# Kernel optimization log

Measured on AMD Instinct MI355X. Metric: run time of the kernel, lower is better.

Reference implementation:

```python
import jax, jax.numpy as jnp
import numpy as np

B, N, C, H, M = 2, 32768, 256, 8, 64
D = C // H  # 32
EPS = 1e-5


def layernorm(x, g, b):
    mu = x.mean(-1, keepdims=True)
    var = ((x - mu) ** 2).mean(-1, keepdims=True)
    return (x - mu) * jax.lax.rsqrt(var + EPS) * g + b


def setup_inputs() -> dict:
    key = jax.random.key(0)
    ks = jax.random.split(key, 12)
    def w(k, shape, fan_in):
        return jax.random.normal(k, shape, jnp.float32) / np.sqrt(fan_in)
    return {
        "x": jax.random.normal(ks[0], (B, N, C), jnp.float32),
        "ln1_g": jnp.ones((C,), jnp.float32),
        "ln1_b": jnp.zeros((C,), jnp.float32),
        "Wfx": w(ks[1], (C, C), C), "bfx": jnp.zeros((C,), jnp.float32),
        "Wx": w(ks[2], (C, C), C), "bx": jnp.zeros((C,), jnp.float32),
        "Wsl": w(ks[3], (D, M), D), "bsl": jnp.zeros((M,), jnp.float32),
        "temp": jnp.full((1, H, 1, 1), 0.5, jnp.float32),
        "Wq": w(ks[4], (D, D), D),
        "Wk": w(ks[5], (D, D), D),
        "Wv": w(ks[6], (D, D), D),
        "Wo": w(ks[7], (C, C), C), "bo": jnp.zeros((C,), jnp.float32),
        "ln2_g": jnp.ones((C,), jnp.float32),
        "ln2_b": jnp.zeros((C,), jnp.float32),
        "W1": w(ks[8], (C, 4 * C), C), "b1": jnp.zeros((4 * C,), jnp.float32),
        "W2": w(ks[9], (4 * C, C), 4 * C), "b2": jnp.zeros((C,), jnp.float32),
    }


def reference(x, ln1_g, ln1_b, Wfx, bfx, Wx, bx, Wsl, bsl, temp,
              Wq, Wk, Wv, Wo, bo, ln2_g, ln2_b, W1, b1, W2, b2):
    scale = D ** -0.5
    h = layernorm(x, ln1_g, ln1_b)
    # projections -> (B,H,N,D)
    fx_mid = (h @ Wfx + bfx).reshape(B, N, H, D).transpose(0, 2, 1, 3)
    x_mid = (h @ Wx + bx).reshape(B, N, H, D).transpose(0, 2, 1, 3)
    # slice routing: (B,H,N,M)
    logits = (x_mid @ Wsl + bsl) / jnp.clip(temp, 0.1, None)
    sw = jax.nn.softmax(logits, axis=-1)
    slice_norm = jnp.clip(sw.sum(axis=2), 1e-5, None)  # (B,H,M)
    slice_token = jnp.einsum('bhnd,bhnm->bhmd', fx_mid, sw) / slice_norm[..., None]
    # small attention over M slices
    q = slice_token @ Wq
    k = slice_token @ Wk
    v = slice_token @ Wv
    attn = jax.nn.softmax(jnp.einsum('bhmd,bhgd->bhmg', q, k) * scale, axis=-1)
    out_slice = jnp.einsum('bhmg,bhgd->bhmd', attn, v)
    # scatter back to N tokens
    out = jnp.einsum('bhmd,bhnm->bhnd', out_slice, sw)
    out = out.transpose(0, 2, 1, 3).reshape(B, N, C) @ Wo + bo
    x = x + out
    h2 = layernorm(x, ln2_g, ln2_b)
    ffn = jax.nn.gelu(h2 @ W1 + b1, approximate=False) @ W2 + b2
    return x + ffn
```

## Files before the change

### kernel.cpp

```cpp
#include <hip/hip_runtime.h>
#include <hip/hip_bf16.h>

typedef float f32x4 __attribute__((ext_vector_type(4)));
typedef short bf16x8 __attribute__((ext_vector_type(8)));
typedef short short4v __attribute__((ext_vector_type(4)));

constexpr int kB = 2, kN = 32768, kC = 256, kH = 8, kD = 32, kM = 64;
constexpr int kT = kB * kN;

__device__ __forceinline__ float b2f(short s) {
    unsigned u = ((unsigned)(unsigned short)s) << 16;
    return __builtin_bit_cast(float, u);
}
__device__ __forceinline__ short f2b(float f) {
    __hip_bfloat16 h = __float2bfloat16(f);
    return __builtin_bit_cast(short, h);
}
__device__ __forceinline__ float gelu_fast(float x) {
    float x2 = x * x;
    float g2 = x * (2.3022042f + 0.10295342f * x2);
#if __has_builtin(__builtin_amdgcn_exp2f)
    float em = __builtin_amdgcn_exp2f(-g2);
#else
    float em = exp2f(-g2);
#endif
#if __has_builtin(__builtin_amdgcn_rcpf)
    return x * __builtin_amdgcn_rcpf(1.0f + em);
#else
    return x / (1.0f + em);
#endif
}

#if __has_builtin(__builtin_amdgcn_global_load_lds)
__device__ __forceinline__ void gld16(const void* g, void* l) {
    __builtin_amdgcn_global_load_lds((__attribute__((address_space(1))) void*)g,
                                     (__attribute__((address_space(3))) void*)l, 16, 0, 0);
}
#else
__device__ __forceinline__ void gld16(const void* g, void* l) {
    *(bf16x8*)l = *(const bf16x8*)g;
}
#endif

__global__ __launch_bounds__(256) void prep_wt(const float* __restrict__ W,
                                               short* __restrict__ Wt, int K, int N) {
    __shared__ float t[32][33];
    int k0 = blockIdx.x * 32, n0 = blockIdx.y * 32;
    int tx = threadIdx.x & 31, ty = threadIdx.x >> 5;
#pragma unroll
    for (int r = 0; r < 32; r += 8)
        t[ty + r][tx] = W[(size_t)(k0 + ty + r) * N + n0 + tx];
    __syncthreads();
#pragma unroll
    for (int r = 0; r < 32; r += 8)
        Wt[(size_t)(n0 + ty + r) * K + k0 + tx] = f2b(t[tx][ty + r]);
}

__global__ __launch_bounds__(256) void prep_pack(const short* __restrict__ src,
                                                 short* __restrict__ dst, int K, int KT) {
    int g = blockIdx.x * 256 + threadIdx.x;
    int frag = g >> 6, lane = g & 63;
    int nt = frag / KT, kt = frag - nt * KT;
    const short* s = &src[(size_t)(nt * 16 + (lane & 15)) * K + kt * 32 + (lane >> 4) * 8];
    *(bf16x8*)&dst[(size_t)frag * 512 + lane * 8] = *(const bf16x8*)s;
}

__global__ __launch_bounds__(256) void prep_wxsl(const float* __restrict__ Wx,
                                                 const float* __restrict__ Wsl,
                                                 const float* __restrict__ bx,
                                                 const float* __restrict__ bsl,
                                                 short* __restrict__ wxsl_t,
                                                 float* __restrict__ bxsl) {
    int n = blockIdx.x;
    int h = n >> 6, m = n & 63;
    int c = threadIdx.x;
    float s = 0.f;
#pragma unroll 8
    for (int dd = 0; dd < 32; ++dd)
        s += Wx[(size_t)c * 256 + h * 32 + dd] * Wsl[dd * 64 + m];
    wxsl_t[(size_t)n * 256 + c] = f2b(s);
    if (c == 0) {
        float bs = bsl[m];
        for (int dd = 0; dd < 32; ++dd) bs += bx[h * 32 + dd] * Wsl[dd * 64 + m];
        bxsl[n] = bs;
    }
}

template <bool IN_BF16>
__global__ __launch_bounds__(256) void ln_kernel(const void* __restrict__ xin,
                                                 const float* __restrict__ g,
                                                 const float* __restrict__ bb,
                                                 short* __restrict__ out) {
    int row = blockIdx.x * 4 + (threadIdx.x >> 6);
    int lane = threadIdx.x & 63;
    float v[4];
    if constexpr (IN_BF16) {
        short4v s = *((const short4v*)((const short*)xin + (size_t)row * kC) + lane);
#pragma unroll
        for (int j = 0; j < 4; ++j) v[j] = b2f(s[j]);
    } else {
        f32x4 s = *((const f32x4*)((const float*)xin + (size_t)row * kC) + lane);
#pragma unroll
        for (int j = 0; j < 4; ++j) v[j] = s[j];
    }
    float sum = v[0] + v[1] + v[2] + v[3];
#pragma unroll
    for (int o = 32; o; o >>= 1) sum += __shfl_xor(sum, o);
    float mu = sum * (1.0f / 256.0f);
    float c[4];
    float s2 = 0.f;
#pragma unroll
    for (int j = 0; j < 4; ++j) { c[j] = v[j] - mu; s2 += c[j] * c[j]; }
#pragma unroll
    for (int o = 32; o; o >>= 1) s2 += __shfl_xor(s2, o);
    float inv = rsqrtf(s2 * (1.0f / 256.0f) + 1e-5f);
    f32x4 gv = *((const f32x4*)g + lane);
    f32x4 bv = *((const f32x4*)bb + lane);
    short4v o;
#pragma unroll
    for (int j = 0; j < 4; ++j) o[j] = f2b(c[j] * inv * gv[j] + bv[j]);
    *((short4v*)(out + (size_t)row * kC) + lane) = o;
}

__global__ __launch_bounds__(256) void wo_gemm(const short* __restrict__ A,
                                               const short* __restrict__ Bt,
                                               const float* __restrict__ bias,
                                               const float* __restrict__ res,
                                               short* __restrict__ Cout) {
    __shared__ __align__(16) short smem[2 * 128 * 64];
    short* As = smem;
    short* Bs = smem + 128 * 64;
    const int tid = threadIdx.x;
    const int lane = tid & 63;
    const int w = tid >> 6, wr = w >> 1, wc = w & 1;
    const int bm = blockIdx.x * 128, bn = blockIdx.y * 128;
    const int l15 = lane & 15, l16 = lane >> 4;
    f32x4 acc[4][4] = {};
    for (int k0 = 0; k0 < 256; k0 += 64) {
        __syncthreads();
#pragma unroll
        for (int l = 0; l < 4; ++l) {
            int li = tid + l * 256;
            int r = li >> 3, s = li & 7;
            int kof = k0 + ((s ^ (r & 7)) << 3);
            gld16(&A[(size_t)(bm + r) * 256 + kof], &As[li * 8]);
            gld16(&Bt[(size_t)(bn + r) * 256 + kof], &Bs[li * 8]);
        }
        __syncthreads();
#pragma unroll
        for (int ks = 0; ks < 2; ++ks) {
            bf16x8 av[4], bv[4];
            int q = ks * 4 + l16;
#pragma unroll
            for (int mi = 0; mi < 4; ++mi) {
                int row = wr * 64 + mi * 16 + l15;
                av[mi] = *(const bf16x8*)(&As[row * 64 + ((q ^ (row & 7)) << 3)]);
            }
#pragma unroll
            for (int ni = 0; ni < 4; ++ni) {
                int row = wc * 64 + ni * 16 + l15;
                bv[ni] = *(const bf16x8*)(&Bs[row * 64 + ((q ^ (row & 7)) << 3)]);
            }
#pragma unroll
            for (int mi = 0; mi < 4; ++mi)
#pragma unroll
                for (int ni = 0; ni < 4; ++ni)
                    acc[mi][ni] = __builtin_amdgcn_mfma_f32_16x16x32_bf16(
                        av[mi], bv[ni], acc[mi][ni], 0, 0, 0);
        }
    }
    __syncthreads();
    char* cs = (char*)smem;
#pragma unroll
    for (int mi = 0; mi < 4; ++mi)
#pragma unroll
        for (int ni = 0; ni < 4; ++ni) {
            int col = wc * 64 + ni * 16 + l15;
            float bcol = bias[bn + col];
#pragma unroll
            for (int r = 0; r < 4; ++r) {
                int row = wr * 64 + mi * 16 + l16 * 4 + r;
                float v = acc[mi][ni][r] + bcol +
                          res[(size_t)(bm + row) * 256 + bn + col];
                *(short*)(cs + row * 256 + ((col * 2) ^ ((row & 7) << 4))) = f2b(v);
            }
        }
    __syncthreads();
#pragma unroll
    for (int pass = 0; pass < 8; ++pass) {
        int row = pass * 16 + (tid >> 4), chunk = tid & 15;
        bf16x8 v = *(const bf16x8*)(cs + row * 256 + ((chunk * 16) ^ ((row & 7) << 4)));
        *(bf16x8*)&Cout[(size_t)(bm + row) * 256 + bn + chunk * 8] = v;
    }
}

__global__ __launch_bounds__(256) void proj_dual(const short* __restrict__ A,
                                                 const short* __restrict__ Bt,
                                                 const float* __restrict__ bfx,
                                                 const float* __restrict__ bxsl,
                                                 short* __restrict__ fxout,
                                                 short* __restrict__ Lout) {
    __shared__ __align__(16) short smem[2 * 128 * 64];
    short* As = smem;
    short* Bs = smem + 128 * 64;
    const int tid = threadIdx.x;
    const int lane = tid & 63;
    const int w = tid >> 6, wr = w >> 1, wc = w & 1;
    const int bm = blockIdx.x * 128, bn = blockIdx.y * 128;
    const int l15 = lane & 15, l16 = lane >> 4;
    f32x4 acc[4][4] = {};
    for (int k0 = 0; k0 < 256; k0 += 64) {
        __syncthreads();
#pragma unroll
        for (int l = 0; l < 4; ++l) {
            int li = tid + l * 256;
            int r = li >> 3, s = li & 7;
            int kof = k0 + ((s ^ (r & 7)) << 3);
            gld16(&A[(size_t)(bm + r) * 256 + kof], &As[li * 8]);
            gld16(&Bt[(size_t)(bn + r) * 256 + kof], &Bs[li * 8]);
        }
        __syncthreads();
#pragma unroll
        for (int ks = 0; ks < 2; ++ks) {
            bf16x8 av[4], bv[4];
            int q = ks * 4 + l16;
#pragma unroll
            for (int mi = 0; mi < 4; ++mi) {
                int row = wr * 64 + mi * 16 + l15;
                av[mi] = *(const bf16x8*)(&As[row * 64 + ((q ^ (row & 7)) << 3)]);
            }
#pragma unroll
            for (int ni = 0; ni < 4; ++ni) {
                int row = wc * 64 + ni * 16 + l15;
                bv[ni] = *(const bf16x8*)(&Bs[row * 64 + ((q ^ (row & 7)) << 3)]);
            }
#pragma unroll
            for (int mi = 0; mi < 4; ++mi)
#pragma unroll
                for (int ni = 0; ni < 4; ++ni)
                    acc[mi][ni] = __builtin_amdgcn_mfma_f32_16x16x32_bf16(
                        av[mi], bv[ni], acc[mi][ni], 0, 0, 0);
        }
    }
    __syncthreads();
    char* cs = (char*)smem;
#pragma unroll
    for (int mi = 0; mi < 4; ++mi)
#pragma unroll
        for (int ni = 0; ni < 4; ++ni) {
            int col = wc * 64 + ni * 16 + l15;
            int gcol = bn + col;
            float bcol = (gcol < 256) ? bfx[gcol] : bxsl[gcol - 256];
#pragma unroll
            for (int r = 0; r < 4; ++r) {
                int row = wr * 64 + mi * 16 + l16 * 4 + r;
                *(short*)(cs + row * 256 + ((col * 2) ^ ((row & 7) << 4))) =
                    f2b(acc[mi][ni][r] + bcol);
            }
        }
    __syncthreads();
    const bool isfx = (bn < 256);
#pragma unroll
    for (int pass = 0; pass < 8; ++pass) {
        int row = pass * 16 + (tid >> 4), chunk = tid & 15;
        bf16x8 v = *(const bf16x8*)(cs + row * 256 + ((chunk * 16) ^ ((row & 7) << 4)));
        if (isfx)
            *(bf16x8*)&fxout[(size_t)(bm + row) * 256 + bn + chunk * 8] = v;
        else
            *(bf16x8*)&Lout[(size_t)(bm + row) * 512 + (bn - 256) + chunk * 8] = v;
    }
}

__global__ __launch_bounds__(256, 2) void ffn_fused(const short* __restrict__ h2,
                                                    const short* __restrict__ xres,
                                                    const short* __restrict__ w1p,
                                                    const short* __restrict__ w2p,
                                                    const float* __restrict__ b1,
                                                    const float* __restrict__ b2,
                                                    float* __restrict__ out) {
    __shared__ __align__(16) short As[64 * 256];
    __shared__ __align__(16) short mids[2][64 * 128];
    const int tid = threadIdx.x;
    const int lane = tid & 63, w = tid >> 6;
    const int l15 = lane & 15, l16 = lane >> 4;
    const int bm = blockIdx.x * 64;
#pragma unroll
    for (int l = 0; l < 8; ++l) {
        int li = tid + l * 256;
        int r = li >> 5, s = li & 31;
        gld16(&h2[(size_t)(bm + r) * 256 + ((s ^ (r & 7)) << 3)], &As[li * 8]);
    }
    __syncthreads();
    f32x4 acc2[4][4] = {};
    f32x4 accm[2][4];

#define FFN_GEMM1(jc)                                                                     \
    {                                                                                     \
        _Pragma("unroll") for (int tj = 0; tj < 4; ++tj) {                                \
            accm[0][tj] = f32x4{0.f, 0.f, 0.f, 0.f};                                      \
            accm[1][tj] = f32x4{0.f, 0.f, 0.f, 0.f};                                      \
        }                                                                                 \
        const short* wp0 = &w1p[(size_t)(((jc)*8 + w * 2) * 8) * 512 + lane * 8];         \
        _Pragma("unroll") for (int ks = 0; ks < 8; ++ks) {                                \
            bf16x8 aw0 = *(const bf16x8*)(wp0 + ks * 512);                                \
            bf16x8 aw1 = *(const bf16x8*)(wp0 + (8 + ks) * 512);                          \
            _Pragma("unroll") for (int tj = 0; tj < 4; ++tj) {                            \
                int row = tj * 16 + l15;                                                  \
                int q = ks * 4 + l16;                                                     \
                bf16x8 bh = *(const bf16x8*)&As[row * 256 + ((q ^ (row & 7)) << 3)];      \
                accm[0][tj] =                                                             \
                    __builtin_amdgcn_mfma_f32_16x16x32_bf16(aw0, bh, accm[0][tj], 0, 0, 0); \
                accm[1][tj] =                                                             \
                    __builtin_amdgcn_mfma_f32_16x16x32_bf16(aw1, bh, accm[1][tj], 0, 0, 0); \
            }                                                                             \
        }                                                                                 \
    }

#define FFN_WRITE(jc)                                                                     \
    {                                                                                     \
        _Pragma("unroll") for (int mcf = 0; mcf < 2; ++mcf) {                             \
            int mc0 = w * 32 + mcf * 16 + l16 * 4;                                        \
            f32x4 bc1 = *(const f32x4*)&b1[(jc)*128 + mc0];                               \
            _Pragma("unroll") for (int tj = 0; tj < 4; ++tj) {                            \
                int token = tj * 16 + l15;                                                \
                short4v pk;                                                               \
                _Pragma("unroll") for (int r = 0; r < 4; ++r)                             \
                    pk[r] = f2b(gelu_fast(accm[mcf][tj][r] + bc1[r]));                    \
                *(short4v*)((char*)mids[(jc)&1] + token * 256 +                           \
                            ((mc0 * 2) ^ ((token & 7) << 4))) = pk;                       \
            }                                                                             \
        }                                                                                 \
    }

#define FFN_GEMM2(jc)                                                                     \
    {                                                                                     \
        _Pragma("unroll") for (int ks = 0; ks < 4; ++ks) {                                \
            int q = ks * 4 + l16;                                                         \
            bf16x8 am[4];                                                                 \
            _Pragma("unroll") for (int mi = 0; mi < 4; ++mi) {                            \
                int row = mi * 16 + l15;                                                  \
                am[mi] = *(const bf16x8*)((const char*)mids[(jc)&1] + row * 256 +         \
                                          ((q * 16) ^ ((row & 7) << 4)));                 \
            }                                                                             \
            _Pragma("unroll") for (int ni = 0; ni < 4; ++ni) {                            \
                bf16x8 bv = *(const bf16x8*)&w2p[(size_t)((w * 4 + ni) * 32 + (jc)*4 +    \
                                                          ks) *                           \
                                                     512 +                                \
                                                 lane * 8];                               \
                _Pragma("unroll") for (int mi = 0; mi < 4; ++mi)                          \
                    acc2[mi][ni] = __builtin_amdgcn_mfma_f32_16x16x32_bf16(               \
                        am[mi], bv, acc2[mi][ni], 0, 0, 0);                               \
            }                                                                             \
        }                                                                                 \
    }

    FFN_GEMM1(0);
#pragma unroll
    for (int jc = 0; jc < 8; ++jc) {
        __syncthreads();
        if (jc > 0) FFN_GEMM2(jc - 1);
        FFN_WRITE(jc);
        if (jc < 7) FFN_GEMM1(jc + 1);
    }
    __syncthreads();
    FFN_GEMM2(7);
#undef FFN_GEMM1
#undef FFN_WRITE
#undef FFN_GEMM2

#pragma unroll
    for (int mi = 0; mi < 4; ++mi)
#pragma unroll
        for (int ni = 0; ni < 4; ++ni) {
            int col = w * 64 + ni * 16 + l15;
            float bc2 = b2[col];
#pragma unroll
            for (int r = 0; r < 4; ++r) {
                size_t row = (size_t)bm + mi * 16 + l16 * 4 + r;
                out[row * 256 + col] = acc2[mi][ni][r] + bc2 + b2f(xres[row * 256 + col]);
            }
        }
}

__global__ __launch_bounds__(256) void fused_slice(const short* __restrict__ L,
                                                   const short* __restrict__ fx,
                                                   const float* __restrict__ temp,
                                                   float* __restrict__ stoken,
                                                   float* __restrict__ snorm) {
    int h = blockIdx.y;
    int t0g = blockIdx.x * 2048;
    int b = t0g >> 15;
    int tid = threadIdx.x;
    int lane = tid & 63, w = tid >> 6;
    int l15 = lane & 15, l16 = lane >> 4;
    __shared__ __align__(16) char smem[57344];
    float inv_t = 1.0f / fmaxf(temp[h], 0.1f);
    const int tt2 = tid * 2;
#pragma unroll
    for (int r = 0; r < 16; ++r) {
        int row = 32 + r;
        *(short*)(smem + 32768 + row * 512 + (tt2 ^ ((row & 7) << 4))) =
            (r == 0) ? (short)0x3F80 : (short)0;
    }
    f32x4 acc[4][3] = {};
    const int swz = (l15 & 7) << 4;
    const int abase = l15 * 512;
    for (int sub = 0; sub < 8; ++sub) {
        __syncthreads();
        int t = t0g + sub * 256 + tid;
        float lg[64];
        const short* Lp = &L[(size_t)t * 512 + h * 64];
#pragma unroll
        for (int mv = 0; mv < 8; ++mv) {
            bf16x8 v = *(const bf16x8*)(Lp + mv * 8);
#pragma unroll
            for (int j = 0; j < 8; ++j) lg[mv * 8 + j] = b2f(v[j]) * inv_t;
        }
        float mx = -1e30f;
#pragma unroll
        for (int m = 0; m < 64; ++m) mx = fmaxf(mx, lg[m]);
        float sum = 0.f;
#pragma unroll
        for (int m = 0; m < 64; ++m) { lg[m] = expf(lg[m] - mx); sum += lg[m]; }
        float inv = 1.0f / sum;
#pragma unroll
        for (int m = 0; m < 64; ++m)
            *(short*)(smem + m * 512 + (tt2 ^ ((m & 7) << 4))) = f2b(lg[m] * inv);
        const short* fxp = &fx[(size_t)t * 256 + h * 32];
#pragma unroll
        for (int mv = 0; mv < 4; ++mv) {
            bf16x8 v = *(const bf16x8*)(fxp + mv * 8);
#pragma unroll
            for (int j = 0; j < 8; ++j)
                *(short*)(smem + 32768 + (mv * 8 + j) * 512 + (tt2 ^ (j << 4))) = v[j];
        }
        __syncthreads();
#pragma unroll
        for (int ks = 0; ks < 2; ++ks) {
            int off = ((w * 8 + ks * 4 + l16) * 16) ^ swz;
            bf16x8 a0 = *(const bf16x8*)(smem + abase + off);
            bf16x8 a1 = *(const bf16x8*)(smem + abase + 8192 + off);
            bf16x8 a2 = *(const bf16x8*)(smem + abase + 16384 + off);
            bf16x8 a3 = *(const bf16x8*)(smem + abase + 24576 + off);
            bf16x8 b0 = *(const bf16x8*)(smem + 32768 + abase + off);
            bf16x8 b1 = *(const bf16x8*)(smem + 32768 + abase + 8192 + off);
            bf16x8 b2v = *(const bf16x8*)(smem + 32768 + abase + 16384 + off);
            acc[0][0] = __builtin_amdgcn_mfma_f32_16x16x32_bf16(a0, b0, acc[0][0], 0, 0, 0);
            acc[0][1] = __builtin_amdgcn_mfma_f32_16x16x32_bf16(a0, b1, acc[0][1], 0, 0, 0);
            acc[0][2] = __builtin_amdgcn_mfma_f32_16x16x32_bf16(a0, b2v, acc[0][2], 0, 0, 0);
            acc[1][0] = __builtin_amdgcn_mfma_f32_16x16x32_bf16(a1, b0, acc[1][0], 0, 0, 0);
            acc[1][1] = __builtin_amdgcn_mfma_f32_16x16x32_bf16(a1, b1, acc[1][1], 0, 0, 0);
            acc[1][2] = __builtin_amdgcn_mfma_f32_16x16x32_bf16(a1, b2v, acc[1][2], 0, 0, 0);
            acc[2][0] = __builtin_amdgcn_mfma_f32_16x16x32_bf16(a2, b0, acc[2][0], 0, 0, 0);
            acc[2][1] = __builtin_amdgcn_mfma_f32_16x16x32_bf16(a2, b1, acc[2][1], 0, 0, 0);
            acc[2][2] = __builtin_amdgcn_mfma_f32_16x16x32_bf16(a2, b2v, acc[2][2], 0, 0, 0);
            acc[3][0] = __builtin_amdgcn_mfma_f32_16x16x32_bf16(a3, b0, acc[3][0], 0, 0, 0);
            acc[3][1] = __builtin_amdgcn_mfma_f32_16x16x32_bf16(a3, b1, acc[3][1], 0, 0, 0);
            acc[3][2] = __builtin_amdgcn_mfma_f32_16x16x32_bf16(a3, b2v, acc[3][2], 0, 0, 0);
        }
    }
    __syncthreads();
    float* red = (float*)smem;
#pragma unroll
    for (int mi = 0; mi < 4; ++mi)
#pragma unroll
        for (int ni = 0; ni < 3; ++ni)
#pragma unroll
            for (int r = 0; r < 4; ++r)
                red[w * 3072 + (mi * 16 + l16 * 4 + r) * 48 + ni * 16 + l15] =
                    acc[mi][ni][r];
    __syncthreads();
    for (int e = tid; e < 3072; e += 256) {
        float s = red[e] + red[3072 + e] + red[6144 + e] + red[9216 + e];
        int m = e / 48, n = e - m * 48;
        if (n < 32)
            atomicAdd(&stoken[(size_t)((b * 8 + h) * 64 + m) * 32 + n], s);
        else if (n == 32)
            atomicAdd(&snorm[(b * 8 + h) * 64 + m], s);
    }
}

__global__ __launch_bounds__(256) void slice_attn_kernel(const float* __restrict__ stoken,
                                                         const float* __restrict__ snorm,
                                                         const float* __restrict__ Wq,
                                                         const float* __restrict__ Wk,
                                                         const float* __restrict__ Wv,
                                                         float* __restrict__ oslice) {
    int bh = blockIdx.x;
    int tid = threadIdx.x;
    int m = tid & 63, grp = tid >> 6;
    __shared__ float st_s[64][33];
    __shared__ float q_s[64][33];
    __shared__ float k_s[64][33];
    __shared__ float v_s[64][33];
    __shared__ float w_s[3][32][32];
    __shared__ float sc_s[64][65];
    __shared__ float nrm_s[64];
    for (int i = tid; i < 3072; i += 256) {
        const float* W = (i < 1024) ? Wq : (i < 2048 ? Wk : Wv);
        int r = i & 1023;
        w_s[i >> 10][r >> 5][r & 31] = W[r];
    }
    if (tid < 64) nrm_s[tid] = 1.0f / fmaxf(snorm[bh * 64 + tid], 1e-5f);
    for (int i = tid; i < 512; i += 256) {
        int mm = i >> 3, dq = (i & 7) << 2;
        f32x4 v = *(const f32x4*)&stoken[(size_t)bh * 2048 + mm * 32 + dq];
        *(f32x4*)&st_s[mm][dq] = v;
    }
    __syncthreads();
    {
        int d0 = grp * 8;
        float qr[8] = {}, kr[8] = {}, vr[8] = {};
#pragma unroll
        for (int dd = 0; dd < 32; ++dd) {
            float s = st_s[m][dd];
#pragma unroll
            for (int j = 0; j < 8; ++j) {
                qr[j] += s * w_s[0][dd][d0 + j];
                kr[j] += s * w_s[1][dd][d0 + j];
                vr[j] += s * w_s[2][dd][d0 + j];
            }
        }
        float nm = nrm_s[m];
#pragma unroll
        for (int j = 0; j < 8; ++j) {
            q_s[m][d0 + j] = qr[j] * nm;
            k_s[m][d0 + j] = kr[j] * nm;
            v_s[m][d0 + j] = vr[j] * nm;
        }
    }
    __syncthreads();
    {
#pragma unroll
        for (int gg = 0; gg < 16; ++gg) {
            int g = grp * 16 + gg;
            float s = 0.f;
#pragma unroll
            for (int dd = 0; dd < 32; ++dd) s += q_s[m][dd] * k_s[g][dd];
            sc_s[m][g] = s * 0.17677669529663687f;
        }
    }
    __syncthreads();
    if (tid < 64) {
        float mx = -1e30f;
#pragma unroll
        for (int g = 0; g < 64; ++g) mx = fmaxf(mx, sc_s[tid][g]);
        float sum = 0.f;
#pragma unroll
        for (int g = 0; g < 64; ++g) {
            float e = expf(sc_s[tid][g] - mx);
            sc_s[tid][g] = e;
            sum += e;
        }
        float inv = 1.0f / sum;
#pragma unroll
        for (int g = 0; g < 64; ++g) sc_s[tid][g] *= inv;
    }
    __syncthreads();
    {
        int d0 = grp * 8;
        float o[8] = {};
#pragma unroll
        for (int g = 0; g < 64; ++g) {
            float p = sc_s[m][g];
#pragma unroll
            for (int j = 0; j < 8; ++j) o[j] += p * v_s[g][d0 + j];
        }
#pragma unroll
        for (int j = 0; j < 8; ++j)
            oslice[(size_t)bh * 2048 + m * 32 + d0 + j] = o[j];
    }
}

__global__ __launch_bounds__(256) void scatter_mfma(const short* __restrict__ L,
                                                    const float* __restrict__ oslice,
                                                    const float* __restrict__ temp,
                                                    short* __restrict__ y) {
    int h = blockIdx.y;
    int t0 = blockIdx.x * 256;
    int b = t0 >> 15;
    int tid = threadIdx.x;
    int lane = tid & 63, w = tid >> 6;
    int l15 = lane & 15, l16 = lane >> 4;
    __shared__ __align__(16) char smem[36864];
    float inv_t = 1.0f / fmaxf(temp[h], 0.1f);
    const float* osp = &oslice[(size_t)(b * 8 + h) * 2048];
    for (int i = tid; i < 2048; i += 256) {
        int m = i >> 5, d = i & 31;
        *(short*)(smem + 32768 + d * 128 + ((2 * m) ^ ((d & 7) << 4))) = f2b(osp[m * 32 + d]);
    }
    float lg[64];
    const short* Lp = &L[(size_t)(t0 + tid) * 512 + h * 64];
#pragma unroll
    for (int mv = 0; mv < 8; ++mv) {
        bf16x8 v = *(const bf16x8*)(Lp + mv * 8);
#pragma unroll
        for (int j = 0; j < 8; ++j) lg[mv * 8 + j] = b2f(v[j]) * inv_t;
    }
    float mx = -1e30f;
#pragma unroll
    for (int m = 0; m < 64; ++m) mx = fmaxf(mx, lg[m]);
    float sum = 0.f;
#pragma unroll
    for (int m = 0; m < 64; ++m) { lg[m] = expf(lg[m] - mx); sum += lg[m]; }
    float inv = 1.0f / sum;
    int tswz = (tid & 7) << 4;
#pragma unroll
    for (int jm = 0; jm < 8; ++jm) {
        bf16x8 o;
#pragma unroll
        for (int j = 0; j < 8; ++j) o[j] = f2b(lg[jm * 8 + j] * inv);
        *(bf16x8*)(smem + tid * 128 + ((jm * 16) ^ tswz)) = o;
    }
    __syncthreads();
    const int swz = (l15 & 7) << 4;
    f32x4 acc[4][2] = {};
#pragma unroll
    for (int ks = 0; ks < 2; ++ks) {
        int off = ((ks * 4 + l16) * 16) ^ swz;
        bf16x8 b0 = *(const bf16x8*)(smem + 32768 + l15 * 128 + off);
        bf16x8 b1 = *(const bf16x8*)(smem + 32768 + (16 + l15) * 128 + off);
#pragma unroll
        for (int i = 0; i < 4; ++i) {
            bf16x8 a = *(const bf16x8*)(smem + (w * 64 + i * 16 + l15) * 128 + off);
            acc[i][0] = __builtin_amdgcn_mfma_f32_16x16x32_bf16(a, b0, acc[i][0], 0, 0, 0);
            acc[i][1] = __builtin_amdgcn_mfma_f32_16x16x32_bf16(a, b1, acc[i][1], 0, 0, 0);
        }
    }
#pragma unroll
    for (int i = 0; i < 4; ++i)
#pragma unroll
        for (int ni = 0; ni < 2; ++ni)
#pragma unroll
            for (int r = 0; r < 4; ++r) {
                int tr = w * 64 + i * 16 + l16 * 4 + r;
                y[(size_t)(t0 + tr) * 256 + h * 32 + ni * 16 + l15] = f2b(acc[i][ni][r]);
            }
}

extern "C" void kernel_launch(void* const* d_in, const int* in_sizes, int n_in,
                              void* d_out, int out_size, void* d_ws, size_t ws_size,
                              hipStream_t stream) {
    (void)in_sizes; (void)n_in; (void)out_size; (void)ws_size;
    const float* x    = (const float*)d_in[0];
    const float* ln1g = (const float*)d_in[1];
    const float* ln1b = (const float*)d_in[2];
    const float* Wfx  = (const float*)d_in[3];
    const float* bfx  = (const float*)d_in[4];
    const float* Wx   = (const float*)d_in[5];
    const float* bx   = (const float*)d_in[6];
    const float* Wsl  = (const float*)d_in[7];
    const float* bsl  = (const float*)d_in[8];
    const float* temp = (const float*)d_in[9];
    const float* Wq   = (const float*)d_in[10];
    const float* Wk   = (const float*)d_in[11];
    const float* Wv   = (const float*)d_in[12];
    const float* Wo   = (const float*)d_in[13];
    const float* bo   = (const float*)d_in[14];
    const float* ln2g = (const float*)d_in[15];
    const float* ln2b = (const float*)d_in[16];
    const float* W1   = (const float*)d_in[17];
    const float* b1   = (const float*)d_in[18];
    const float* W2   = (const float*)d_in[19];
    const float* b2   = (const float*)d_in[20];
    float* out = (float*)d_out;

    constexpr size_t SLOT = (size_t)kT * kC * 2;
    char* ws = (char*)d_ws;
    short* S0 = (short*)(ws);
    short* S1 = (short*)(ws + SLOT);
    char*  S3 = ws + 3 * SLOT;
    short* wfx_t  = (short*)(S3);
    short* wxsl_t = (short*)(S3 + 131072);
    short* wo_t   = (short*)(S3 + 393216);
    short* w1_t   = (short*)(S3 + 524288);
    short* w2_t   = (short*)(S3 + 1048576);
    float* bxsl   = (float*)(S3 + 1572864);
    float* stoken = (float*)(S3 + 1574912);
    float* snorm  = (float*)(S3 + 1705984);
    float* oslice = (float*)(S3 + 1710080);
    short* w1p    = (short*)(S3 + 1841152);
    short* w2p    = (short*)(S3 + 2365440);

    short* h    = S0;
    short* fx   = S1;
    short* y    = S0;
    short* xres = S1;
    short* h2   = S0;
    short* Lbuf = (short*)d_out;

    prep_wt<<<dim3(8, 8), 256, 0, stream>>>(Wfx, wfx_t, 256, 256);
    prep_wt<<<dim3(8, 8), 256, 0, stream>>>(Wo, wo_t, 256, 256);
    prep_wt<<<dim3(8, 32), 256, 0, stream>>>(W1, w1_t, 256, 1024);
    prep_wt<<<dim3(32, 8), 256, 0, stream>>>(W2, w2_t, 1024, 256);
    prep_wxsl<<<512, 256, 0, stream>>>(Wx, Wsl, bx, bsl, wxsl_t, bxsl);
    prep_pack<<<128, 256, 0, stream>>>(w1_t, w1p, 256, 8);
    prep_pack<<<128, 256, 0, stream>>>(w2_t, w2p, 1024, 32);
    hipMemsetAsync(stoken, 0, 131072 + 4096, stream);

    ln_kernel<false><<<kT / 4, 256, 0, stream>>>(x, ln1g, ln1b, h);
    proj_dual<<<dim3(kT / 128, 6), 256, 0, stream>>>(h, wfx_t, bfx, bxsl, fx, Lbuf);
    fused_slice<<<dim3(kT / 2048, kH), 256, 0, stream>>>(Lbuf, fx, temp, stoken, snorm);
    slice_attn_kernel<<<kB * kH, 256, 0, stream>>>(stoken, snorm, Wq, Wk, Wv, oslice);
    scatter_mfma<<<dim3(kT / 256, kH), 256, 0, stream>>>(Lbuf, oslice, temp, y);
    wo_gemm<<<dim3(kT / 128, 2), 256, 0, stream>>>(y, wo_t, bo, x, xres);
    ln_kernel<true><<<kT / 4, 256, 0, stream>>>(xres, ln2g, ln2b, h2);
    ffn_fused<<<kT / 64, 256, 0, stream>>>(h2, xres, w1p, w2p, b1, b2, out);
}
```

Measured before the change: 305.5 us.

## Restructure scatter kernel to cover all heads per token tile and coalesce output stores

```diff
diff --git a/kernel.cpp b/kernel.cpp
--- a/kernel.cpp
+++ b/kernel.cpp
@@ -572,70 +572,92 @@
     }
 }
 
-__global__ __launch_bounds__(256) void scatter_mfma(const short* __restrict__ L,
+__global__ __launch_bounds__(256) void scatter_coal(const short* __restrict__ L,
                                                     const float* __restrict__ oslice,
                                                     const float* __restrict__ temp,
                                                     short* __restrict__ y) {
-    int h = blockIdx.y;
-    int t0 = blockIdx.x * 256;
-    int b = t0 >> 15;
-    int tid = threadIdx.x;
-    int lane = tid & 63, w = tid >> 6;
-    int l15 = lane & 15, l16 = lane >> 4;
-    __shared__ __align__(16) char smem[36864];
-    float inv_t = 1.0f / fmaxf(temp[h], 0.1f);
-    const float* osp = &oslice[(size_t)(b * 8 + h) * 2048];
-    for (int i = tid; i < 2048; i += 256) {
-        int m = i >> 5, d = i & 31;
-        *(short*)(smem + 32768 + d * 128 + ((2 * m) ^ ((d & 7) << 4))) = f2b(osp[m * 32 + d]);
-    }
-    float lg[64];
-    const short* Lp = &L[(size_t)(t0 + tid) * 512 + h * 64];
-#pragma unroll
-    for (int mv = 0; mv < 8; ++mv) {
-        bf16x8 v = *(const bf16x8*)(Lp + mv * 8);
-#pragma unroll
-        for (int j = 0; j < 8; ++j) lg[mv * 8 + j] = b2f(v[j]) * inv_t;
-    }
-    float mx = -1e30f;
-#pragma unroll
-    for (int m = 0; m < 64; ++m) mx = fmaxf(mx, lg[m]);
-    float sum = 0.f;
-#pragma unroll
-    for (int m = 0; m < 64; ++m) { lg[m] = expf(lg[m] - mx); sum += lg[m]; }
-    float inv = 1.0f / sum;
-    int tswz = (tid & 7) << 4;
-#pragma unroll
-    for (int jm = 0; jm < 8; ++jm) {
-        bf16x8 o;
-#pragma unroll
-        for (int j = 0; j < 8; ++j) o[j] = f2b(lg[jm * 8 + j] * inv);
-        *(bf16x8*)(smem + tid * 128 + ((jm * 16) ^ tswz)) = o;
-    }
-    __syncthreads();
-    const int swz = (l15 & 7) << 4;
-    f32x4 acc[4][2] = {};
-#pragma unroll
-    for (int ks = 0; ks < 2; ++ks) {
-        int off = ((ks * 4 + l16) * 16) ^ swz;
-        bf16x8 b0 = *(const bf16x8*)(smem + 32768 + l15 * 128 + off);
-        bf16x8 b1 = *(const bf16x8*)(smem + 32768 + (16 + l15) * 128 + off);
-#pragma unroll
-        for (int i = 0; i < 4; ++i) {
-            bf16x8 a = *(const bf16x8*)(smem + (w * 64 + i * 16 + l15) * 128 + off);
-            acc[i][0] = __builtin_amdgcn_mfma_f32_16x16x32_bf16(a, b0, acc[i][0], 0, 0, 0);
-            acc[i][1] = __builtin_amdgcn_mfma_f32_16x16x32_bf16(a, b1, acc[i][1], 0, 0, 0);
-        }
-    }
-#pragma unroll
-    for (int i = 0; i < 4; ++i)
-#pragma unroll
-        for (int ni = 0; ni < 2; ++ni)
-#pragma unroll
-            for (int r = 0; r < 4; ++r) {
-                int tr = w * 64 + i * 16 + l16 * 4 + r;
-                y[(size_t)(t0 + tr) * 256 + h * 32 + ni * 16 + l15] = f2b(acc[i][ni][r]);
-            }
+    __shared__ __align__(16) char ys[32768];
+    __shared__ __align__(16) char sw_s[2][8192];
+    __shared__ __align__(16) char os_t[2][4096];
+    const int tid = threadIdx.x;
+    const int lane = tid & 63, w = tid >> 6;
+    const int l15 = lane & 15, l16 = lane >> 4;
+    const int t0 = blockIdx.x * 64;
+    const int b = t0 >> 15;
+    for (int rnd = 0; rnd < 4; ++rnd) {
+        int h0 = rnd * 2;
+        __syncthreads();
+        if (tid < 128) {
+            int hh = tid >> 6, token = tid & 63;
+            int hsel = h0 + hh;
+            float inv_t = 1.0f / fmaxf(temp[hsel], 0.1f);
+            const short* Lp = &L[(size_t)(t0 + token) * 512 + hsel * 64];
+            float lg[64];
+#pragma unroll
+            for (int mv = 0; mv < 8; ++mv) {
+                bf16x8 v = *(const bf16x8*)(Lp + mv * 8);
+#pragma unroll
+                for (int j = 0; j < 8; ++j) lg[mv * 8 + j] = b2f(v[j]) * inv_t;
+            }
+            float mx = -1e30f;
+#pragma unroll
+            for (int m = 0; m < 64; ++m) mx = fmaxf(mx, lg[m]);
+            float sum = 0.f;
+#pragma unroll
+            for (int m = 0; m < 64; ++m) { lg[m] = expf(lg[m] - mx); sum += lg[m]; }
+            float inv = 1.0f / sum;
+            int tswz = (token & 7) << 4;
+#pragma unroll
+            for (int jm = 0; jm < 8; ++jm) {
+                bf16x8 o;
+#pragma unroll
+                for (int j = 0; j < 8; ++j) o[j] = f2b(lg[jm * 8 + j] * inv);
+                *(bf16x8*)(sw_s[hh] + token * 128 + ((jm * 16) ^ tswz)) = o;
+            }
+        } else {
+            for (int i = tid - 128; i < 4096; i += 128) {
+                int hh = i >> 11, j = i & 2047;
+                int m = j >> 5, d = j & 31;
+                *(short*)(os_t[hh] + d * 128 + ((2 * m) ^ ((d & 7) << 4))) =
+                    f2b(oslice[(size_t)(b * 8 + h0 + hh) * 2048 + j]);
+            }
+        }
+        __syncthreads();
+        int trow = w * 16 + l15;
+        int tswz2 = (trow & 7) << 4;
+#pragma unroll
+        for (int hh = 0; hh < 2; ++hh) {
+            f32x4 acc[2] = {};
+#pragma unroll
+            for (int ks = 0; ks < 2; ++ks) {
+                int off = (ks * 4 + l16) * 16;
+                bf16x8 bt = *(const bf16x8*)(sw_s[hh] + trow * 128 + (off ^ tswz2));
+                bf16x8 a0 = *(const bf16x8*)(os_t[hh] + l15 * 128 + (off ^ ((l15 & 7) << 4)));
+                bf16x8 a1 = *(const bf16x8*)(os_t[hh] + (16 + l15) * 128 +
+                                             (off ^ (((16 + l15) & 7) << 4)));
+                acc[0] = __builtin_amdgcn_mfma_f32_16x16x32_bf16(a0, bt, acc[0], 0, 0, 0);
+                acc[1] = __builtin_amdgcn_mfma_f32_16x16x32_bf16(a1, bt, acc[1], 0, 0, 0);
+            }
+#pragma unroll
+            for (int df = 0; df < 2; ++df) {
+                short4v pk;
+#pragma unroll
+                for (int r = 0; r < 4; ++r) pk[r] = f2b(acc[df][r]);
+                *(short4v*)(ys + (size_t)trow * 512 +
+                            (((h0 + hh) * 64 + df * 32 + l16 * 8) ^ tswz2)) = pk;
+            }
+        }
+    }
+    __syncthreads();
+    {
+        int row = tid >> 5, chunk = tid & 31;
+#pragma unroll
+        for (int pass = 0; pass < 8; ++pass) {
+            int rr = pass * 8 + row;
+            bf16x8 v = *(const bf16x8*)(ys + rr * 512 + ((chunk * 16) ^ ((rr & 7) << 4)));
+            *(bf16x8*)&y[(size_t)(t0 + rr) * 256 + chunk * 8] = v;
+        }
+    }
 }
 
 extern "C" void kernel_launch(void* const* d_in, const int* in_sizes, int n_in,
@@ -702,7 +724,7 @@
     proj_dual<<<dim3(kT / 128, 6), 256, 0, stream>>>(h, wfx_t, bfx, bxsl, fx, Lbuf);
     fused_slice<<<dim3(kT / 2048, kH), 256, 0, stream>>>(Lbuf, fx, temp, stoken, snorm);
     slice_attn_kernel<<<kB * kH, 256, 0, stream>>>(stoken, snorm, Wq, Wk, Wv, oslice);
-    scatter_mfma<<<dim3(kT / 256, kH), 256, 0, stream>>>(Lbuf, oslice, temp, y);
+    scatter_coal<<<kT / 64, 256, 0, stream>>>(Lbuf, oslice, temp, y);
     wo_gemm<<<dim3(kT / 128, 2), 256, 0, stream>>>(y, wo_t, bo, x, xres);
     ln_kernel<true><<<kT / 4, 256, 0, stream>>>(xres, ln2g, ln2b, h2);
     ffn_fused<<<kT / 64, 256, 0, stream>>>(h2, xres, w1p, w2p, b1, b2, out);
```

Measured after the change: 319.4 us. +4.5%, slower.
